# Performance work log

Hardware: AMD Instinct MI355X
Metric: run time of the kernel (lower is better)

## Reference

```python
import jax, jax.numpy as jnp
import numpy as np

B, H, W, C = 16, 32, 32, 256
N = H * W


def setup_inputs() -> dict:
    key = jax.random.key(0)
    ks = jax.random.split(key, 8)
    x = jax.random.normal(ks[0], (B, H, W, C), dtype=jnp.float32)
    # nn.LazyLinear(C): weight (C, C), bias (C,)
    scale = 1.0 / np.sqrt(C)
    Wq = jax.random.uniform(ks[1], (C, C), jnp.float32, -scale, scale)
    bq = jax.random.uniform(ks[2], (C,), jnp.float32, -scale, scale)
    Wk = jax.random.uniform(ks[3], (C, C), jnp.float32, -scale, scale)
    bk = jax.random.uniform(ks[4], (C,), jnp.float32, -scale, scale)
    Wv = jax.random.uniform(ks[5], (C, C), jnp.float32, -scale, scale)
    bv = jax.random.uniform(ks[6], (C,), jnp.float32, -scale, scale)
    # torch.randn(H, H*W, W)
    Wp = jax.random.normal(ks[7], (H, N, W), dtype=jnp.float32)
    return {"x": x, "Wq": Wq, "bq": bq, "Wk": Wk, "bk": bk,
            "Wv": Wv, "bv": bv, "Wp": Wp}


def reference(x, Wq, bq, Wk, bk, Wv, bv, Wp):
    b, h, w, c = x.shape
    n = h * w
    # Linear projections (torch Linear: x @ W^T + b), flatten spatial dims to N tokens
    q = (jnp.einsum('bhwc,dc->bhwd', x, Wq) + bq).reshape(b, n, c)
    k = (jnp.einsum('bhwc,dc->bhwd', x, Wk) + bk).reshape(b, n, c)
    v = (jnp.einsum('bhwc,dc->bhwd', x, Wv) + bv).reshape(b, n, c)
    # Unscaled attention over the N spatial tokens (no 1/sqrt(C) in the original)
    scores = jnp.einsum('bnc,bmc->bnm', q, k)          # (B, N, N)
    attn = jax.nn.softmax(scores, axis=-1)
    qkv = jnp.einsum('bnm,bmc->bnc', attn, v)           # (B, N, C)
    # z = (qkv^T [B,1,C,N] @ Wp [H,N,W]).transpose(-2,-1) -> (B, H, W, C)
    z = jnp.einsum('bnc,hnw->bhwc', qkv, Wp)
    return z
```

## Files before the change

kernel.cpp:

```cpp
#include <hip/hip_runtime.h>
#include <hip/hip_bf16.h>

#define BB 16
#define NN 1024
#define CC 256

typedef __attribute__((ext_vector_type(8))) short bf16x8;
typedef __attribute__((ext_vector_type(4))) short s16x4;
typedef __attribute__((ext_vector_type(4))) float f32x4;

#define GPTR(p) ((const __attribute__((address_space(1))) void*)(p))
#define LPTR(p) ((__attribute__((address_space(3))) void*)(p))

__device__ __forceinline__ unsigned short f2bf(float f) {
  union { float f; unsigned u; } v; v.f = f;
  unsigned r = v.u + 0x7FFFu + ((v.u >> 16) & 1u);
  return (unsigned short)(r >> 16);
}

__device__ __forceinline__ bf16x8 pack8(f32x4 a, f32x4 b) {
  bf16x8 o;
  o[0] = (short)f2bf(a[0]); o[1] = (short)f2bf(a[1]);
  o[2] = (short)f2bf(a[2]); o[3] = (short)f2bf(a[3]);
  o[4] = (short)f2bf(b[0]); o[5] = (short)f2bf(b[1]);
  o[6] = (short)f2bf(b[2]); o[7] = (short)f2bf(b[3]);
  return o;
}

template <int BIAS_MODE, int F32OUT>
__global__ __launch_bounds__(256) void gemm_tile(
    const unsigned short* __restrict__ A, int lda, long sA,
    const unsigned short* __restrict__ Bt, int ldb, long sB,
    const float* __restrict__ bias,
    void* __restrict__ Out, int ldo, long sO, int K) {
  __shared__ unsigned short As[2 * 128 * 32];
  __shared__ unsigned short Bs[2 * 64 * 32];
  int b = blockIdx.x;
  int m0 = blockIdx.y * 128;
  int n0 = blockIdx.z * 64;
  int t = threadIdx.x;
  int w = t >> 6, lane = t & 63;
  int wm = (w >> 1) * 64, wn = (w & 1) * 32;
  int r = lane & 15, g = lane >> 4;

  const unsigned short* Ab = A + (long)b * sA;
  const unsigned short* Bb = Bt + (long)b * sB;

  int srow = t >> 2;
  int scol = (t & 3) * 8;

  f32x4 acc[4][2];
#pragma unroll
  for (int i = 0; i < 4; i++)
#pragma unroll
    for (int j = 0; j < 2; j++) acc[i][j] = (f32x4){0.f, 0.f, 0.f, 0.f};

  for (int k0 = 0; k0 < K; k0 += 64) {
    __syncthreads();
#pragma unroll
    for (int kh = 0; kh < 2; kh++) {
#pragma unroll
      for (int jj = 0; jj < 2; jj++) {
        __builtin_amdgcn_global_load_lds(
            GPTR(Ab + (long)(m0 + srow + jj * 64) * lda + k0 + kh * 32 + scol),
            LPTR(&As[kh * 4096 + jj * 2048 + t * 8]), 16, 0, 0);
      }
      __builtin_amdgcn_global_load_lds(
          GPTR(Bb + (long)(n0 + srow) * ldb + k0 + kh * 32 + scol),
          LPTR(&Bs[kh * 2048 + t * 8]), 16, 0, 0);
    }
    __syncthreads();
#pragma unroll
    for (int kh = 0; kh < 2; kh++) {
      bf16x8 af[4], bfr[2];
#pragma unroll
      for (int ti = 0; ti < 4; ti++)
        af[ti] = *(const bf16x8*)&As[kh * 4096 + (wm + ti * 16 + r) * 32 + g * 8];
#pragma unroll
      for (int tj = 0; tj < 2; tj++)
        bfr[tj] = *(const bf16x8*)&Bs[kh * 2048 + (wn + tj * 16 + r) * 32 + g * 8];
#pragma unroll
      for (int ti = 0; ti < 4; ti++)
#pragma unroll
        for (int tj = 0; tj < 2; tj++)
          acc[ti][tj] = __builtin_amdgcn_mfma_f32_16x16x32_bf16(af[ti], bfr[tj], acc[ti][tj], 0, 0, 0);
    }
  }

#pragma unroll
  for (int ti = 0; ti < 4; ti++) {
#pragma unroll
    for (int tj = 0; tj < 2; tj++) {
      int col = n0 + wn + tj * 16 + r;
      float bc = (BIAS_MODE == 1) ? bias[col] : 0.0f;
#pragma unroll
      for (int rr = 0; rr < 4; rr++) {
        int row = m0 + wm + ti * 16 + g * 4 + rr;
        float val = acc[ti][tj][rr] + bc;
        long oidx = (long)b * sO + (long)row * ldo + col;
        if (F32OUT)
          ((float*)Out)[oidx] = val;
        else
          ((unsigned short*)Out)[oidx] = f2bf(val);
      }
    }
  }
}

__global__ __launch_bounds__(256) void gemm_qkv(
    const float* __restrict__ x,
    const float* __restrict__ Wq, const float* __restrict__ Wk,
    const float* __restrict__ Wv,
    const float* __restrict__ bq, const float* __restrict__ bk,
    const float* __restrict__ bv,
    const float* __restrict__ Wp,
    unsigned short* __restrict__ Qb, unsigned short* __restrict__ Kb,
    unsigned short* __restrict__ Vtb, unsigned short* __restrict__ Amat) {
  __shared__ unsigned short As[2 * 128 * 32];
  __shared__ unsigned short Bs[2 * 128 * 32];
  __shared__ float tile[32][33];

  if (blockIdx.z == 6) {
    int id = blockIdx.x * 8 + blockIdx.y;
#pragma unroll 1
    for (int u = 0; u < 8; u++) {
      int wb = id * 8 + u;
      int h = wb >> 5;
      int n0w = (wb & 31) * 32;
#pragma unroll
      for (int j = 0; j < 4; j++) {
        int idx = threadIdx.x + j * 256;
        int a = idx >> 5, wc = idx & 31;
        tile[a][wc] = Wp[(size_t)h * (NN * 32) + (size_t)(n0w + a) * 32 + wc];
      }
      __syncthreads();
#pragma unroll
      for (int j = 0; j < 4; j++) {
        int idx = threadIdx.x + j * 256;
        int wc = idx >> 5, a = idx & 31;
        Amat[(size_t)(h * 32 + wc) * NN + n0w + a] = f2bf(tile[a][wc]);
      }
      __syncthreads();
    }
    return;
  }

  int b = blockIdx.x;
  int m0 = blockIdx.y * 128;
  int n0 = blockIdx.z * 128;
  int t = threadIdx.x;
  int w = t >> 6, lane = t & 63;
  int wm = (w >> 1) * 64, wn = (w & 1) * 64;
  int r = lane & 15, g = lane >> 4;

  const float* Ab = x + (long)b * NN * CC;
  int srow = t >> 2;
  int scol = (t & 3) * 8;

  const float* Wsel[2];
  int wrow[2];
#pragma unroll
  for (int jj = 0; jj < 2; jj++) {
    int nbase = n0 + jj * 64;
    int seg = nbase >> 8;
    Wsel[jj] = (seg == 0) ? Wq : (seg == 1 ? Wk : Wv);
    wrow[jj] = (nbase + srow) & 255;
  }

  f32x4 acc[4][4];
#pragma unroll
  for (int i = 0; i < 4; i++)
#pragma unroll
    for (int j = 0; j < 4; j++) acc[i][j] = (f32x4){0.f, 0.f, 0.f, 0.f};

  f32x4 pa[4][2];
#pragma unroll
  for (int kh = 0; kh < 2; kh++)
#pragma unroll
    for (int jj = 0; jj < 2; jj++) {
      const float* src = Ab + (long)(m0 + srow + jj * 64) * CC + kh * 32 + scol;
      pa[kh * 2 + jj][0] = *(const f32x4*)src;
      pa[kh * 2 + jj][1] = *(const f32x4*)(src + 4);
    }

  for (int k0 = 0; k0 < CC; k0 += 64) {
    __syncthreads();
#pragma unroll
    for (int kh = 0; kh < 2; kh++) {
#pragma unroll
      for (int jj = 0; jj < 2; jj++) {
        const float* wsrc = Wsel[jj] + (long)wrow[jj] * CC + k0 + kh * 32 + scol;
        f32x4 b0 = *(const f32x4*)wsrc;
        f32x4 b1 = *(const f32x4*)(wsrc + 4);
        *(bf16x8*)&Bs[kh * 4096 + jj * 2048 + t * 8] = pack8(b0, b1);
        *(bf16x8*)&As[kh * 4096 + jj * 2048 + t * 8] =
            pack8(pa[kh * 2 + jj][0], pa[kh * 2 + jj][1]);
      }
    }
    __syncthreads();
    if (k0 < CC - 64) {
#pragma unroll
      for (int kh = 0; kh < 2; kh++)
#pragma unroll
        for (int jj = 0; jj < 2; jj++) {
          const float* src =
              Ab + (long)(m0 + srow + jj * 64) * CC + k0 + 64 + kh * 32 + scol;
          pa[kh * 2 + jj][0] = *(const f32x4*)src;
          pa[kh * 2 + jj][1] = *(const f32x4*)(src + 4);
        }
    }
#pragma unroll
    for (int kh = 0; kh < 2; kh++) {
      bf16x8 af[4], bfr[4];
#pragma unroll
      for (int ti = 0; ti < 4; ti++)
        af[ti] = *(const bf16x8*)&As[kh * 4096 + (wm + ti * 16 + r) * 32 + g * 8];
#pragma unroll
      for (int tj = 0; tj < 4; tj++)
        bfr[tj] = *(const bf16x8*)&Bs[kh * 4096 + (wn + tj * 16 + r) * 32 + g * 8];
#pragma unroll
      for (int ti = 0; ti < 4; ti++)
#pragma unroll
        for (int tj = 0; tj < 4; tj++)
          acc[ti][tj] = __builtin_amdgcn_mfma_f32_16x16x32_bf16(af[ti], bfr[tj], acc[ti][tj], 0, 0, 0);
    }
  }

  int sege = (n0 + wn) >> 8;
  const float* bsel = (sege == 0) ? bq : (sege == 1 ? bk : bv);
  int seg = n0 >> 8;
#pragma unroll
  for (int ti = 0; ti < 4; ti++) {
#pragma unroll
    for (int tj = 0; tj < 4; tj++) {
      int col = n0 + wn + tj * 16 + r;
      int c = col & 255;
      float bc = bsel[c];
#pragma unroll
      for (int rr = 0; rr < 4; rr++) {
        int row = m0 + wm + ti * 16 + g * 4 + rr;
        float val = acc[ti][tj][rr] + bc;
        long base = (long)b * NN * CC;
        if (seg == 0) {
          Qb[base + (long)row * CC + c] = f2bf(val);
        } else if (seg == 1) {
          Kb[base + ((long)(c >> 5) * NN + row) * 32 + (c & 31)] = f2bf(val);
        } else {
          Vtb[base + ((((long)(c >> 4) * 128 + (row >> 3)) * 16 + (c & 15)) * 8 + (row & 7))] = f2bf(val);
        }
      }
    }
  }
}

__global__ __launch_bounds__(512, 2) void attn_fused(
    const unsigned short* __restrict__ Q,
    const unsigned short* __restrict__ Kt,
    const unsigned short* __restrict__ Vt,
    unsigned short* __restrict__ QKVt) {
  __shared__ unsigned short ShBuf[64 * 1024];
  __shared__ float red[8][64];
  int b = blockIdx.x;
  int n0 = blockIdx.y * 64;
  int t = threadIdx.x;
  int w = t >> 6, lane = t & 63;
  int r = lane & 15, g = lane >> 4;

  const unsigned short* kslab = Kt + (long)b * NN * CC + w * 128 * 32;
  unsigned short* wbuf0 = &ShBuf[w * 4096];
  unsigned short* wbuf1 = &ShBuf[32768 + w * 4096];

  const unsigned short* qbase = Q + ((long)b * NN + n0 + r) * CC + g * 8;

#pragma unroll
  for (int j = 0; j < 8; j++)
    __builtin_amdgcn_global_load_lds(GPTR(kslab + j * 512 + lane * 8),
                                     LPTR(wbuf0 + j * 512 + lane * 8), 16, 0, 0);
  bf16x8 qa[4];
#pragma unroll
  for (int rt = 0; rt < 4; rt++)
    qa[rt] = *(const bf16x8*)(qbase + rt * 16 * CC);

  f32x4 acc[4][8];
#pragma unroll
  for (int i = 0; i < 4; i++)
#pragma unroll
    for (int j = 0; j < 8; j++) acc[i][j] = (f32x4){0.f, 0.f, 0.f, 0.f};

#pragma unroll
  for (int kk = 0; kk < 8; kk++) {
    unsigned short* cur = (kk & 1) ? wbuf1 : wbuf0;
    unsigned short* nxt = (kk & 1) ? wbuf0 : wbuf1;
    if (kk < 7) {
      const unsigned short* src = kslab + (long)(kk + 1) * (NN * 32);
#pragma unroll
      for (int j = 0; j < 8; j++)
        __builtin_amdgcn_global_load_lds(GPTR(src + j * 512 + lane * 8),
                                         LPTR(nxt + j * 512 + lane * 8), 16, 0, 0);
      asm volatile("s_waitcnt vmcnt(8)" ::: "memory");
    } else {
      asm volatile("s_waitcnt vmcnt(0)" ::: "memory");
    }
    __builtin_amdgcn_sched_barrier(0);
    bf16x8 qn[4];
    if (kk < 7) {
#pragma unroll
      for (int rt = 0; rt < 4; rt++)
        qn[rt] = *(const bf16x8*)(qbase + (kk + 1) * 32 + rt * 16 * CC);
    }
    __builtin_amdgcn_s_setprio(1);
#pragma unroll
    for (int ct = 0; ct < 8; ct++) {
      bf16x8 kf = *(const bf16x8*)&cur[(ct * 16 + r) * 32 + g * 8];
#pragma unroll
      for (int rt = 0; rt < 4; rt++)
        acc[rt][ct] = __builtin_amdgcn_mfma_f32_16x16x32_bf16(qa[rt], kf, acc[rt][ct], 0, 0, 0);
    }
    __builtin_amdgcn_s_setprio(0);
    if (kk < 7) {
#pragma unroll
      for (int rt = 0; rt < 4; rt++) qa[rt] = qn[rt];
    }
    __builtin_amdgcn_sched_barrier(0);
  }

  const unsigned short* vbase = Vt + (long)b * NN * CC;
  int cw = w * 32;
  bf16x8 brp[2];
#pragma unroll
  for (int bt = 0; bt < 2; bt++) {
    long vidx = (((long)((cw >> 4) + bt) * 128 + g) * 16 + r) * 8;
    brp[bt] = *(const bf16x8*)(vbase + vidx);
  }
  __builtin_amdgcn_sched_barrier(0);

  float mrow[4][4];
#pragma unroll
  for (int rt = 0; rt < 4; rt++) {
#pragma unroll
    for (int rr = 0; rr < 4; rr++) {
      float m = acc[rt][0][rr];
#pragma unroll
      for (int ct = 1; ct < 8; ct++) m = fmaxf(m, acc[rt][ct][rr]);
#pragma unroll
      for (int d = 1; d < 16; d <<= 1) m = fmaxf(m, __shfl_xor(m, d, 64));
      mrow[rt][rr] = m;
    }
  }
  if (r == 0) {
#pragma unroll
    for (int rt = 0; rt < 4; rt++)
#pragma unroll
      for (int rr = 0; rr < 4; rr++)
        red[w][rt * 16 + g * 4 + rr] = mrow[rt][rr];
  }
  __syncthreads();
#pragma unroll
  for (int rt = 0; rt < 4; rt++) {
#pragma unroll
    for (int rr = 0; rr < 4; rr++) {
      int row = rt * 16 + g * 4 + rr;
      float m = red[0][row];
#pragma unroll
      for (int w2 = 1; w2 < 8; w2++) m = fmaxf(m, red[w2][row]);
      mrow[rt][rr] = m;
    }
  }
  __syncthreads();
  float ssum[4][4];
#pragma unroll
  for (int rt = 0; rt < 4; rt++) {
#pragma unroll
    for (int rr = 0; rr < 4; rr++) {
      float s = 0.f;
#pragma unroll
      for (int ct = 0; ct < 8; ct++) {
        float e = exp2f((acc[rt][ct][rr] - mrow[rt][rr]) * 1.44269504088896f);
        acc[rt][ct][rr] = e;
        s += e;
      }
#pragma unroll
      for (int d = 1; d < 16; d <<= 1) s += __shfl_xor(s, d, 64);
      ssum[rt][rr] = s;
    }
  }
  if (r == 0) {
#pragma unroll
    for (int rt = 0; rt < 4; rt++)
#pragma unroll
      for (int rr = 0; rr < 4; rr++)
        red[w][rt * 16 + g * 4 + rr] = ssum[rt][rr];
  }
  __syncthreads();
#pragma unroll
  for (int rt = 0; rt < 4; rt++) {
#pragma unroll
    for (int rr = 0; rr < 4; rr++) {
      int prow = rt * 16 + g * 4 + rr;
      float s = 0.f;
#pragma unroll
      for (int w2 = 0; w2 < 8; w2++) s += red[w2][prow];
      float inv = 1.0f / s;
      int sw = prow & 7;
#pragma unroll
      for (int ct = 0; ct < 8; ct++) {
        int col = w * 128 + ct * 16 + r;
        int chunk = (col >> 3) ^ sw;
        ShBuf[prow * 1024 + chunk * 8 + (col & 7)] = f2bf(acc[rt][ct][rr] * inv);
      }
    }
  }
  __syncthreads();

  f32x4 o[4][2];
#pragma unroll
  for (int i = 0; i < 4; i++)
#pragma unroll
    for (int j = 0; j < 2; j++) o[i][j] = (f32x4){0.f, 0.f, 0.f, 0.f};

#pragma unroll 4
  for (int m0 = 0; m0 < NN; m0 += 32) {
    bf16x8 ar[4], br[2];
    br[0] = brp[0]; br[1] = brp[1];
    if (m0 + 32 < NN) {
#pragma unroll
      for (int bt = 0; bt < 2; bt++) {
        long vidx = (((long)((cw >> 4) + bt) * 128 + ((m0 + 32) >> 3) + g) * 16 + r) * 8;
        brp[bt] = *(const bf16x8*)(vbase + vidx);
      }
    }
#pragma unroll
    for (int rt = 0; rt < 4; rt++) {
      int prow = rt * 16 + r;
      int chunk = ((m0 >> 3) + g) ^ (prow & 7);
      ar[rt] = *(const bf16x8*)&ShBuf[prow * 1024 + chunk * 8];
    }
    __builtin_amdgcn_s_setprio(1);
#pragma unroll
    for (int rt = 0; rt < 4; rt++)
#pragma unroll
      for (int bt = 0; bt < 2; bt++)
        o[rt][bt] = __builtin_amdgcn_mfma_f32_16x16x32_bf16(ar[rt], br[bt], o[rt][bt], 0, 0, 0);
    __builtin_amdgcn_s_setprio(0);
  }

  unsigned short* obase = QKVt + (long)b * NN * CC;
#pragma unroll
  for (int rt = 0; rt < 4; rt++) {
#pragma unroll
    for (int bt = 0; bt < 2; bt++) {
      int c = cw + bt * 16 + r;
      int n = n0 + rt * 16 + g * 4;
      s16x4 pk;
      pk.x = (short)f2bf(o[rt][bt][0]);
      pk.y = (short)f2bf(o[rt][bt][1]);
      pk.z = (short)f2bf(o[rt][bt][2]);
      pk.w = (short)f2bf(o[rt][bt][3]);
      *(s16x4*)(obase + (long)c * NN + n) = pk;
    }
  }
}

extern "C" void kernel_launch(void* const* d_in, const int* in_sizes, int n_in,
                              void* d_out, int out_size, void* d_ws, size_t ws_size,
                              hipStream_t stream) {
  const float* x  = (const float*)d_in[0];
  const float* Wq = (const float*)d_in[1];
  const float* bq = (const float*)d_in[2];
  const float* Wk = (const float*)d_in[3];
  const float* bk = (const float*)d_in[4];
  const float* Wv = (const float*)d_in[5];
  const float* bv = (const float*)d_in[6];
  const float* Wp = (const float*)d_in[7];
  float* out = (float*)d_out;

  const long BNC = (long)BB * NN * CC;

  char* p = (char*)d_ws;
  unsigned short* Amat  = (unsigned short*)p; p += (long)NN * NN * 2;
  unsigned short* Qb    = (unsigned short*)p; p += BNC * 2;
  unsigned short* Ktb   = (unsigned short*)p; p += BNC * 2;
  unsigned short* Vtb   = (unsigned short*)p; p += BNC * 2;
  unsigned short* QKVt  = (unsigned short*)p; p += BNC * 2;

  gemm_qkv<<<dim3(BB, 8, 7), 256, 0, stream>>>(
      x, Wq, Wk, Wv, bq, bk, bv, Wp, Qb, Ktb, Vtb, Amat);

  attn_fused<<<dim3(BB, NN / 64), 512, 0, stream>>>(Qb, Ktb, Vtb, QKVt);

  gemm_tile<0, 1><<<dim3(BB, 8, 4), 256, 0, stream>>>(
      Amat, NN, 0L, QKVt, NN, (long)NN * CC, nullptr,
      out, CC, (long)NN * CC, NN);
}
```

Baseline: 151.5 us.

## Double-buffer LDS staging in GEMM tile and prefetch weights in QKV projection

The generic bf16 GEMM tile now keeps two LDS buffers and issues the direct-to-LDS global loads for the next K-slice before computing the current one. It waits with a partial vmcnt so those loads overlap with MFMA work. The fused QKV projection kernel now prefetches the fp32 weight rows into registers one step ahead, like the activations, and replaces __syncthreads with explicit barriers plus an lgkmcnt wait. This hides global-load latency at the cost of twice the LDS in the GEMM tile and more registers in the projection kernel, which may lower occupancy.

```diff
diff --git a/kernel.cpp b/kernel.cpp
--- a/kernel.cpp
+++ b/kernel.cpp
@@ -33,8 +33,8 @@
     const unsigned short* __restrict__ Bt, int ldb, long sB,
     const float* __restrict__ bias,
     void* __restrict__ Out, int ldo, long sO, int K) {
-  __shared__ unsigned short As[2 * 128 * 32];
-  __shared__ unsigned short Bs[2 * 64 * 32];
+  __shared__ unsigned short As[2][2 * 128 * 32];
+  __shared__ unsigned short Bs[2][2 * 64 * 32];
   int b = blockIdx.x;
   int m0 = blockIdx.y * 128;
   int n0 = blockIdx.z * 64;
@@ -55,37 +55,52 @@
 #pragma unroll
     for (int j = 0; j < 2; j++) acc[i][j] = (f32x4){0.f, 0.f, 0.f, 0.f};
 
-  for (int k0 = 0; k0 < K; k0 += 64) {
-    __syncthreads();
-#pragma unroll
-    for (int kh = 0; kh < 2; kh++) {
-#pragma unroll
-      for (int jj = 0; jj < 2; jj++) {
-        __builtin_amdgcn_global_load_lds(
-            GPTR(Ab + (long)(m0 + srow + jj * 64) * lda + k0 + kh * 32 + scol),
-            LPTR(&As[kh * 4096 + jj * 2048 + t * 8]), 16, 0, 0);
-      }
-      __builtin_amdgcn_global_load_lds(
-          GPTR(Bb + (long)(n0 + srow) * ldb + k0 + kh * 32 + scol),
-          LPTR(&Bs[kh * 2048 + t * 8]), 16, 0, 0);
-    }
-    __syncthreads();
+#define STAGE_GT(buf, k0)                                                     \
+  do {                                                                        \
+    _Pragma("unroll") for (int kh = 0; kh < 2; kh++) {                        \
+      _Pragma("unroll") for (int jj = 0; jj < 2; jj++) {                      \
+        __builtin_amdgcn_global_load_lds(                                     \
+            GPTR(Ab + (long)(m0 + srow + jj * 64) * lda + (k0) + kh * 32 +    \
+                 scol),                                                       \
+            LPTR(&As[buf][kh * 4096 + jj * 2048 + t * 8]), 16, 0, 0);         \
+      }                                                                       \
+      __builtin_amdgcn_global_load_lds(                                       \
+          GPTR(Bb + (long)(n0 + srow) * ldb + (k0) + kh * 32 + scol),         \
+          LPTR(&Bs[buf][kh * 2048 + t * 8]), 16, 0, 0);                       \
+    }                                                                         \
+  } while (0)
+
+  int nt = K >> 6;
+  STAGE_GT(0, 0);
+  for (int tt = 0; tt < nt; ++tt) {
+    int cb = tt & 1;
+    if (tt < nt - 1) {
+      STAGE_GT(cb ^ 1, (tt + 1) * 64);
+      asm volatile("s_waitcnt vmcnt(6)" ::: "memory");
+    } else {
+      asm volatile("s_waitcnt vmcnt(0)" ::: "memory");
+    }
+    __builtin_amdgcn_sched_barrier(0);
+    __builtin_amdgcn_s_barrier();
+    __builtin_amdgcn_sched_barrier(0);
 #pragma unroll
     for (int kh = 0; kh < 2; kh++) {
       bf16x8 af[4], bfr[2];
 #pragma unroll
       for (int ti = 0; ti < 4; ti++)
-        af[ti] = *(const bf16x8*)&As[kh * 4096 + (wm + ti * 16 + r) * 32 + g * 8];
+        af[ti] = *(const bf16x8*)&As[cb][kh * 4096 + (wm + ti * 16 + r) * 32 + g * 8];
 #pragma unroll
       for (int tj = 0; tj < 2; tj++)
-        bfr[tj] = *(const bf16x8*)&Bs[kh * 2048 + (wn + tj * 16 + r) * 32 + g * 8];
+        bfr[tj] = *(const bf16x8*)&Bs[cb][kh * 2048 + (wn + tj * 16 + r) * 32 + g * 8];
 #pragma unroll
       for (int ti = 0; ti < 4; ti++)
 #pragma unroll
         for (int tj = 0; tj < 2; tj++)
           acc[ti][tj] = __builtin_amdgcn_mfma_f32_16x16x32_bf16(af[ti], bfr[tj], acc[ti][tj], 0, 0, 0);
     }
-  }
+    __builtin_amdgcn_s_barrier();
+  }
+#undef STAGE_GT
 
 #pragma unroll
   for (int ti = 0; ti < 4; ti++) {
@@ -173,42 +188,49 @@
 #pragma unroll
     for (int j = 0; j < 4; j++) acc[i][j] = (f32x4){0.f, 0.f, 0.f, 0.f};
 
-  f32x4 pa[4][2];
+  f32x4 pa[4][2], pw[4][2];
 #pragma unroll
   for (int kh = 0; kh < 2; kh++)
 #pragma unroll
     for (int jj = 0; jj < 2; jj++) {
-      const float* src = Ab + (long)(m0 + srow + jj * 64) * CC + kh * 32 + scol;
-      pa[kh * 2 + jj][0] = *(const f32x4*)src;
-      pa[kh * 2 + jj][1] = *(const f32x4*)(src + 4);
+      const float* asrc = Ab + (long)(m0 + srow + jj * 64) * CC + kh * 32 + scol;
+      pa[kh * 2 + jj][0] = *(const f32x4*)asrc;
+      pa[kh * 2 + jj][1] = *(const f32x4*)(asrc + 4);
+      const float* wsrc = Wsel[jj] + (long)wrow[jj] * CC + kh * 32 + scol;
+      pw[kh * 2 + jj][0] = *(const f32x4*)wsrc;
+      pw[kh * 2 + jj][1] = *(const f32x4*)(wsrc + 4);
     }
 
   for (int k0 = 0; k0 < CC; k0 += 64) {
-    __syncthreads();
-#pragma unroll
-    for (int kh = 0; kh < 2; kh++) {
+    if (k0) __builtin_amdgcn_s_barrier();
+#pragma unroll
+    for (int kh = 0; kh < 2; kh++)
 #pragma unroll
       for (int jj = 0; jj < 2; jj++) {
-        const float* wsrc = Wsel[jj] + (long)wrow[jj] * CC + k0 + kh * 32 + scol;
-        f32x4 b0 = *(const f32x4*)wsrc;
-        f32x4 b1 = *(const f32x4*)(wsrc + 4);
-        *(bf16x8*)&Bs[kh * 4096 + jj * 2048 + t * 8] = pack8(b0, b1);
         *(bf16x8*)&As[kh * 4096 + jj * 2048 + t * 8] =
             pack8(pa[kh * 2 + jj][0], pa[kh * 2 + jj][1]);
-      }
-    }
-    __syncthreads();
+        *(bf16x8*)&Bs[kh * 4096 + jj * 2048 + t * 8] =
+            pack8(pw[kh * 2 + jj][0], pw[kh * 2 + jj][1]);
+      }
     if (k0 < CC - 64) {
 #pragma unroll
       for (int kh = 0; kh < 2; kh++)
 #pragma unroll
         for (int jj = 0; jj < 2; jj++) {
-          const float* src =
+          const float* asrc =
               Ab + (long)(m0 + srow + jj * 64) * CC + k0 + 64 + kh * 32 + scol;
-          pa[kh * 2 + jj][0] = *(const f32x4*)src;
-          pa[kh * 2 + jj][1] = *(const f32x4*)(src + 4);
+          pa[kh * 2 + jj][0] = *(const f32x4*)asrc;
+          pa[kh * 2 + jj][1] = *(const f32x4*)(asrc + 4);
+          const float* wsrc =
+              Wsel[jj] + (long)wrow[jj] * CC + k0 + 64 + kh * 32 + scol;
+          pw[kh * 2 + jj][0] = *(const f32x4*)wsrc;
+          pw[kh * 2 + jj][1] = *(const f32x4*)(wsrc + 4);
         }
     }
+    asm volatile("s_waitcnt lgkmcnt(0)" ::: "memory");
+    __builtin_amdgcn_sched_barrier(0);
+    __builtin_amdgcn_s_barrier();
+    __builtin_amdgcn_sched_barrier(0);
 #pragma unroll
     for (int kh = 0; kh < 2; kh++) {
       bf16x8 af[4], bfr[4];
```

Measured after the change: 149.9 us. Within noise of the previous version (-1.0%).
